# Performance work log

Hardware: AMD Instinct MI355X
Metric: run time of the kernel (lower is better)

The kernel has to match this reference:

```python
import jax, jax.numpy as jnp
import numpy as np
from jax import lax

EPS = 1e-05
Q = 4          # window size (hard-coded in BotBlock)
HEADS = 4
DIM = 16       # bottleneck(64) // heads(4)


def conv3x3(x, w, b):
    # x: [N,C,H,W], w: [O,I,3,3]
    y = lax.conv_general_dilated(x, w, (1, 1), ((1, 1), (1, 1)),
                                 dimension_numbers=('NCHW', 'OIHW', 'NCHW'))
    return y + b[None, :, None, None]


def batchnorm(x, gamma, beta):
    # training-mode BN: batch statistics over (N,H,W), biased variance
    m = jnp.mean(x, axis=(0, 2, 3), keepdims=True)
    v = jnp.var(x, axis=(0, 2, 3), keepdims=True)
    xn = (x - m) * lax.rsqrt(v + EPS)
    return xn * gamma[None, :, None, None] + beta[None, :, None, None]


def rel_to_abs(x):
    # x: [B, H, L, 2L-1] -> [B, H, L, L] via pad/reshape trick
    B, H, L, _ = x.shape
    x = jnp.pad(x, ((0, 0), (0, 0), (0, 0), (0, 1)))          # [B,H,L,2L]
    flat = x.reshape(B, H, -1)                                  # [B,H,2L*L]
    flat = jnp.pad(flat, ((0, 0), (0, 0), (0, L - 1)))
    final = flat.reshape(B, H, L + 1, 2 * L - 1)
    return final[:, :, :L, L - 1:]                              # [B,H,L,L]


def relative_logits_1d(q, rel_k, perm):
    # q: [b, n, h, w, d], rel_k: [2w-1, d]
    b, n, h, w, d = q.shape
    rl = jnp.einsum('bnhwd,md->bnhwm', q, rel_k)
    rl = rl.reshape(b, n * h, w, 2 * w - 1)
    rl = rel_to_abs(rl)                                         # [b, n*h, w, w]
    rl = rl.reshape(b, n, h, w, w)
    rl = jnp.broadcast_to(rl[:, :, :, None], (b, n, h, h, w, w))
    return jnp.transpose(rl, perm)


def rel_pos_attention(q, k, v, rel_w, rel_h):
    # q,k,v: [b, heads, h, w, d]
    b, n, h, w, d = q.shape
    q = q * (d ** -0.5)
    logits = jnp.einsum('bnhwd,bnpqd->bnhwpq', q, k)
    logits = logits + relative_logits_1d(q, rel_w, (0, 1, 2, 4, 3, 5))
    logits = logits + relative_logits_1d(jnp.transpose(q, (0, 1, 3, 2, 4)),
                                         rel_h, (0, 1, 4, 2, 5, 3))
    weights = jax.nn.softmax(logits.reshape(b, n, h, w, h * w), axis=-1)
    weights = weights.reshape(b, n, h, w, h, w)
    out = jnp.einsum('bnhwpq,bnpqd->bhwnd', weights, v)         # [b,h,w,n,d]
    return out.reshape(b, h, w, n * d)                          # fold heads


def setup_inputs() -> dict:
    key = jax.random.key(0)
    ks = jax.random.split(key, 16)
    C_in, C_bot, C_out = 64, 64, 256
    inp = {
        'x': jax.random.normal(ks[0], (2, C_in, 256, 256), jnp.float32),
        'conv1_w': jax.random.normal(ks[1], (C_bot, C_in, 3, 3), jnp.float32) * 0.05,
        'conv1_b': jnp.zeros((C_bot,), jnp.float32),
        'bn1_g': jnp.ones((C_bot,), jnp.float32),
        'bn1_b': jnp.zeros((C_bot,), jnp.float32),
        'wq': jax.random.normal(ks[2], (C_bot, HEADS, DIM), jnp.float32) * 0.01,
        'wk': jax.random.normal(ks[3], (C_bot, HEADS, DIM), jnp.float32) * 0.01,
        'wv': jax.random.normal(ks[4], (C_bot, HEADS, DIM), jnp.float32) * 0.01,
        'rel_w': jax.random.normal(ks[5], (2 * Q - 1, DIM), jnp.float32) * (DIM ** -0.5),
        'rel_h': jax.random.normal(ks[6], (2 * Q - 1, DIM), jnp.float32) * (DIM ** -0.5),
        'bn2_g': jnp.ones((C_bot,), jnp.float32),
        'bn2_b': jnp.zeros((C_bot,), jnp.float32),
        'conv3_w': jax.random.normal(ks[7], (C_out, C_bot, 3, 3), jnp.float32) * 0.05,
        'conv3_b': jnp.zeros((C_out,), jnp.float32),
        # NOTE: original init_zero=True zeros bn3 gamma; we randomize it so the
        # output (and gradients) are non-trivial for kernel correctness checks.
        'bn3_g': jax.random.normal(ks[8], (C_out,), jnp.float32),
        'bn3_b': jnp.zeros((C_out,), jnp.float32),
    }
    return inp


def reference(x, conv1_w, conv1_b, bn1_g, bn1_b, wq, wk, wv, rel_w, rel_h,
              bn2_g, bn2_b, conv3_w, conv3_b, bn3_g, bn3_b):
    N, C, H, W = x.shape
    P_h, P_w = H // Q, W // Q
    # raw memory reinterpretation into 4x4 blocks (matches torch .reshape)
    xb = x.reshape(N * P_h * P_w, C, Q, Q)
    out = jax.nn.relu(batchnorm(conv3x3(xb, conv1_w, conv1_b), bn1_g, bn1_b))
    # GroupPointWise projections: NCHW -> NHWC then einsum
    feat = jnp.transpose(out, (0, 2, 3, 1))                     # [b,h,w,c]
    q = jnp.einsum('bhwc,cnp->bnhwp', feat, wq)
    k = jnp.einsum('bhwc,cnp->bnhwp', feat, wk)
    v = jnp.einsum('bhwc,cnp->bnhwp', feat, wv)
    o = rel_pos_attention(q, k, v, rel_w, rel_h)                # [b,h,w,c]
    o = jnp.transpose(o, (0, 3, 1, 2))                          # NCHW
    o = jax.nn.relu(batchnorm(o, bn2_g, bn2_b))
    o = batchnorm(conv3x3(o, conv3_w, conv3_b), bn3_g, bn3_b)   # no act
    C1 = o.shape[1]
    o = o.reshape(N, C1, H, W)
    return jax.nn.relu(o)
```

## Files before the change

kernel.cpp:

```cpp
#include <hip/hip_runtime.h>
#include <stdint.h>


#define EPSV 1e-5f
#define INV_N (1.0f / 131072.0f)

typedef unsigned short u16;
typedef __attribute__((ext_vector_type(8))) short short8b;
typedef __attribute__((ext_vector_type(4))) float f32x4;

__device__ __forceinline__ u16 f2bf(float f) {
  unsigned u = __float_as_uint(f);
  u += 0x7fffu + ((u >> 16) & 1u);
  return (u16)(u >> 16);
}
__device__ __forceinline__ float bf2f(u16 h) {
  return __uint_as_float((unsigned)h << 16);
}
__device__ __forceinline__ unsigned cvtpk(float lo, float hi) {
  unsigned r;
  asm("v_cvt_pk_bf16_f32 %0, %1, %2" : "=v"(r) : "v"(lo), "v"(hi));
  return r;
}

__device__ __forceinline__ float bn_scale(const float* __restrict__ acc,
                                          const float* __restrict__ gam,
                                          const float* __restrict__ bet,
                                          int C, int c, float& shift) {
  float S = acc[c], S2 = acc[C + c];
  float mean = S * INV_N;
  float var  = S2 * INV_N - mean * mean;
  float rstd = rsqrtf(var + EPSV);
  float sc = gam[c] * rstd;
  shift = bet[c] - mean * sc;
  return sc;
}

__global__ __launch_bounds__(256) void prep_kernel(const float* __restrict__ w1,
                                                   const float* __restrict__ w3,
                                                   const float* __restrict__ wq,
                                                   const float* __restrict__ wk,
                                                   const float* __restrict__ wv,
                                                   const float* __restrict__ relw,
                                                   const float* __restrict__ relh,
                                                   u16* __restrict__ wp1,
                                                   u16* __restrict__ wp3,
                                                   u16* __restrict__ wqkvT) {
  int i = blockIdx.x * 256 + threadIdx.x;
  const int tot1 = 18 * 64 * 40;
  const int tot3 = 9 * 256 * 64;
  if (i < tot1) {
    int ch = i / (64 * 40); int r = i - ch * 64 * 40; int o = r / 40; int kk = r - o * 40;
    float v = 0.f;
    if (kk < 32) { int k = ch * 32 + kk; int tap = k >> 6; int c = k & 63;
                   v = w1[o * 576 + c * 9 + tap]; }
    wp1[i] = f2bf(v);
  } else if (i < tot1 + tot3) {
    int j = i - tot1;
    int tap = j >> 14; int r = j & 16383; int o = r >> 6; int c = r & 63;
    wp3[j] = f2bf(w3[o * 576 + c * 9 + tap]);
  } else if (i < tot1 + tot3 + 192 * 64) {
    int j = i - tot1 - tot3;
    int oc = j >> 6, c = j & 63;
    const float* src = (oc < 64) ? wq : (oc < 128) ? wk : wv;
    wqkvT[j] = f2bf(src[(c << 6) + (oc & 63)]);
  } else if (i < tot1 + tot3 + 192 * 64 + 4096) {
    int j = i - tot1 - tot3 - 192 * 64;
    int c = j & 63; int col = (j >> 6) & 31; int tbl = j >> 11;
    int n = col >> 3, m = col & 7;
    float v = 0.f;
    if (m < 7) {
      const float* rel = tbl ? relh : relw;
#pragma unroll
      for (int d = 0; d < 16; ++d) v += wq[c * 64 + n * 16 + d] * rel[m * 16 + d];
    }
    wqkvT[(192 + tbl * 32 + col) * 64 + c] = f2bf(v);
  }
}

__global__ __launch_bounds__(256) void conv1_kernel(const float* __restrict__ x,
                                                    const u16* __restrict__ wp,
                                                    u16* __restrict__ bufb,
                                                    float* __restrict__ partials1) {
  __shared__ __align__(16) char featA[257 * 128];
  __shared__ __align__(16) char ldsW[2][64 * 80];
  const int t = threadIdx.x;
  const int lane = t & 63, w = t >> 6;
  const int lrow = lane & 15, lk = lane >> 4;
  const int wm = w >> 1, wn = w & 1;
  const size_t Mbase = (size_t)blockIdx.x * 256;

  int rel[9];
  {
    const int pi = lrow >> 2, pj = lrow & 3;
#pragma unroll
    for (int tap = 0; tap < 9; ++tap) {
      const int ti = tap / 3, tj = tap - ti * 3;
      int si = pi + ti - 1, sj = pj + tj - 1;
      bool valid = ((unsigned)si < 4u) && ((unsigned)sj < 4u);
      rel[tap] = valid ? ((si * 4 + sj) << 7) : (1 << 24);
    }
  }

  {
    const int cp = t >> 3, ph = t & 7;
    const int gsw = ((cp >> 2) << 4) | ((cp & 3) << 2);
#pragma unroll
    for (int i = 0; i < 16; ++i) {
      const float* bp = x + Mbase * 64 + i * 1024 + cp * 32 + ph * 2;
      float2 a = *reinterpret_cast<const float2*>(bp);
      float2 b = *reinterpret_cast<const float2*>(bp + 16);
#pragma unroll
      for (int j = 0; j < 2; ++j) {
        const int row = i * 16 + ph * 2 + j;
        unsigned pk = cvtpk(j ? a.y : a.x, j ? b.y : b.x);
        const int byte = row * 128 + (gsw ^ ((row & 7) << 4));
        *reinterpret_cast<unsigned*>(featA + byte) = pk;
      }
    }
  }
  if (t < 8) *reinterpret_cast<uint4*>(featA + 256 * 128 + t * 16) = uint4{0, 0, 0, 0};

  uint4 s0, s1;
  {
    const u16* sp = wp;
    s0 = *reinterpret_cast<const uint4*>(sp + (size_t)t * 8);
    if (t < 64) s1 = *reinterpret_cast<const uint4*>(sp + (size_t)(t + 256) * 8);
    *reinterpret_cast<uint4*>(ldsW[0] + t * 16) = s0;
    if (t < 64) *reinterpret_cast<uint4*>(ldsW[0] + (t + 256) * 16) = s1;
  }
  __syncthreads();

  f32x4 acc[8][2] = {};
#pragma unroll
  for (int chn = 0; chn < 18; ++chn) {
    const int cur = chn & 1;
    const int tap = chn >> 1, kk = chn & 1;
    if (chn + 1 < 18) {
      const u16* sp = wp + (chn + 1) * 2560;
      s0 = *reinterpret_cast<const uint4*>(sp + (size_t)t * 8);
      if (t < 64) s1 = *reinterpret_cast<const uint4*>(sp + (size_t)(t + 256) * 8);
    }
    const int kkg = (kk << 6) | (lk << 4);
    short8b bw[2];
#pragma unroll
    for (int n = 0; n < 2; ++n)
      bw[n] = *reinterpret_cast<const short8b*>(ldsW[cur] + (wn * 32 + n * 16 + lrow) * 80 + lk * 16);
#pragma unroll
    for (int m = 0; m < 8; ++m) {
      int ad = ((wm * 128 + m * 16) << 7) + rel[tap];
      ad = ad < 32768 ? ad : 32768;
      ad += (kkg ^ ((ad >> 3) & 0x70));
      short8b af = *reinterpret_cast<const short8b*>(featA + ad);
#pragma unroll
      for (int n = 0; n < 2; ++n)
        acc[m][n] = __builtin_amdgcn_mfma_f32_16x16x32_bf16(af, bw[n], acc[m][n], 0, 0, 0);
    }
    if (chn + 1 < 18) {
      *reinterpret_cast<uint4*>(ldsW[cur ^ 1] + t * 16) = s0;
      if (t < 64) *reinterpret_cast<uint4*>(ldsW[cur ^ 1] + (t + 256) * 16) = s1;
    }
    __syncthreads();
  }

#pragma unroll
  for (int m = 0; m < 8; ++m) {
    const size_t rowg0 = Mbase + wm * 128 + m * 16 + lk * 4;
#pragma unroll
    for (int n = 0; n < 2; ++n) {
      const int o = wn * 32 + n * 16 + lrow;
#pragma unroll
      for (int r = 0; r < 4; ++r)
        bufb[(rowg0 + r) * 64 + o] = f2bf(acc[m][n][r]);
    }
  }

  float* pst = reinterpret_cast<float*>(featA);
  if (t < 128) pst[t] = 0.f;
  __syncthreads();
#pragma unroll
  for (int n = 0; n < 2; ++n) {
    float s = 0.f, s2 = 0.f;
#pragma unroll
    for (int m = 0; m < 8; ++m)
#pragma unroll
      for (int r = 0; r < 4; ++r) {
        float v = acc[m][n][r];
        s += v; s2 = fmaf(v, v, s2);
      }
    s += __shfl_xor(s, 16); s2 += __shfl_xor(s2, 16);
    s += __shfl_xor(s, 32); s2 += __shfl_xor(s2, 32);
    if (lk == 0) {
      const int o = wn * 32 + n * 16 + lrow;
      atomicAdd(&pst[o], s);
      atomicAdd(&pst[64 + o], s2);
    }
  }
  __syncthreads();
  if (t < 128) partials1[(size_t)blockIdx.x * 128 + t] = pst[t];
}

__global__ __launch_bounds__(256) void reduce12_kernel(const float* __restrict__ p,
                                                       float* __restrict__ acc, int nrows) {
  const int c = blockIdx.x, t = threadIdx.x;
  float s = 0.f;
  for (int i = t; i < nrows; i += 256) s += p[(size_t)i * 128 + c];
#pragma unroll
  for (int off = 32; off > 0; off >>= 1) s += __shfl_down(s, off);
  __shared__ float red[4];
  if ((t & 63) == 0) red[t >> 6] = s;
  __syncthreads();
  if (t == 0) acc[c] = red[0] + red[1] + red[2] + red[3];
}

__global__ __launch_bounds__(256) void attn_kernel(u16* __restrict__ buf,
                                                   const u16* __restrict__ wqkvT,
                                                   const float* __restrict__ acc1,
                                                   const float* __restrict__ g1,
                                                   const float* __restrict__ b1,
                                                   float* __restrict__ partials2) {
  __shared__ float scsh[64][2];
  __shared__ float pstA[128];
  __shared__ __align__(16) u16 feat_l[4][1024];
  __shared__ __align__(16) float qkvf[4][3200];
  __shared__ __align__(16) float relLs[4][1152];
  const int t = threadIdx.x, u = t >> 6, lane = t & 63;
  const size_t b = (size_t)blockIdx.x * 4 + u;
  float* Wf = qkvf[u];
  float* rL = relLs[u];

  if (t < 64) {
    float sh; float sc = bn_scale(acc1, g1, b1, 64, t, sh);
    scsh[t][0] = sc; scsh[t][1] = sh;
  }
  if (t < 128) pstA[t] = 0.f;
  __syncthreads();

  {
    const int pos = lane >> 2, cq = lane & 3;
    const u16* src = buf + b * 1024 + pos * 64 + cq * 16;
    short8b v0 = *reinterpret_cast<const short8b*>(src);
    short8b v1 = *reinterpret_cast<const short8b*>(src + 8);
    float f[16];
#pragma unroll
    for (int j = 0; j < 8; ++j) {
      const int c0 = cq * 16 + j, c1 = cq * 16 + 8 + j;
      f[j]     = fmaxf(fmaf(bf2f((u16)v0[j]), scsh[c0][0], scsh[c0][1]), 0.f);
      f[8 + j] = fmaxf(fmaf(bf2f((u16)v1[j]), scsh[c1][0], scsh[c1][1]), 0.f);
    }
    uint4 q0{cvtpk(f[0], f[1]), cvtpk(f[2], f[3]), cvtpk(f[4], f[5]), cvtpk(f[6], f[7])};
    uint4 q1{cvtpk(f[8], f[9]), cvtpk(f[10], f[11]), cvtpk(f[12], f[13]), cvtpk(f[14], f[15])};
    const int g0 = (cq * 2) ^ (pos & 7), g1g = (cq * 2 + 1) ^ (pos & 7);
    *reinterpret_cast<uint4*>(&feat_l[u][pos * 64 + g0 * 8]) = q0;
    *reinterpret_cast<uint4*>(&feat_l[u][pos * 64 + g1g * 8]) = q1;
  }

  const int dq = lane & 15, lk = lane >> 4;
  short8b afr[2];
#pragma unroll
  for (int ch = 0; ch < 2; ++ch) {
    const int kg = ch * 4 + lk;
    afr[ch] = *reinterpret_cast<const short8b*>(&feat_l[u][dq * 64 + ((kg ^ (dq & 7)) * 8)]);
  }
#pragma unroll
  for (int ct = 0; ct < 16; ++ct) {
    f32x4 d = {0.f, 0.f, 0.f, 0.f};
#pragma unroll
    for (int ch = 0; ch < 2; ++ch) {
      short8b bfr = *reinterpret_cast<const short8b*>(&wqkvT[(ct * 16 + dq) * 64 + ch * 32 + lk * 8]);
      d = __builtin_amdgcn_mfma_f32_16x16x32_bf16(afr[ch], bfr, d, 0, 0, 0);
    }
    if (ct < 4) {
      float* dst = Wf + ct * 272;
#pragma unroll
      for (int r = 0; r < 4; ++r) dst[(lk * 4 + r) * 17 + dq] = d[r] * 0.25f;
    } else if (ct < 12) {
      float* dst = (ct < 8) ? (Wf + 1088 + (ct - 4) * 264) : (Wf + 2144 + (ct - 8) * 264);
      const int cp = dq ^ (lk << 2);
#pragma unroll
      for (int r = 0; r < 4; ++r) dst[(lk * 4 + r) * 16 + cp] = d[r];
    } else {
      const int rc = ct - 12, tbl = rc >> 1;
      const int nn = ((rc & 1) << 1) | (dq >> 3), mm = dq & 7;
      float* dst = rL + tbl * 576 + nn * 144 + mm;
#pragma unroll
      for (int r = 0; r < 4; ++r) dst[(lk * 4 + r) * 9] = d[r] * 0.25f;
    }
  }

  const int n = lk, qp = dq;
  const int qi = qp >> 2, qj = qp & 3;
  float q_[16];
  {
    const float* qb = Wf + n * 272 + qp * 17;
#pragma unroll
    for (int d2 = 0; d2 < 16; ++d2) q_[d2] = qb[d2];
  }
  float rwq[4], rhq[4];
  {
    const float* rw = rL + n * 144 + qp * 9 + (3 - qj);
    const float* rh = rL + 576 + n * 144 + qp * 9 + (3 - qi);
#pragma unroll
    for (int k = 0; k < 4; ++k) { rwq[k] = rw[k]; rhq[k] = rh[k]; }
  }
  float lo[16]; float mx = -1e30f;
  const float* kbase = Wf + 1088 + n * 264;
#pragma unroll
  for (int kp = 0; kp < 16; ++kp) {
    const float4* kr = reinterpret_cast<const float4*>(kbase + kp * 16);
    float s = rwq[kp & 3] + rhq[kp >> 2];
#pragma unroll
    for (int g = 0; g < 4; ++g) {
      float4 kv = kr[g];
      const int lg = (g ^ (kp >> 2)) * 4;
      s = fmaf(q_[lg], kv.x, s); s = fmaf(q_[lg + 1], kv.y, s);
      s = fmaf(q_[lg + 2], kv.z, s); s = fmaf(q_[lg + 3], kv.w, s);
    }
    lo[kp] = s; mx = fmaxf(mx, s);
  }
  float ssum = 0.f;
#pragma unroll
  for (int kp = 0; kp < 16; ++kp) { float e = __expf(lo[kp] - mx); lo[kp] = e; ssum += e; }
  const float inv = 1.0f / ssum;
  float ov[16];
#pragma unroll
  for (int j = 0; j < 16; ++j) ov[j] = 0.f;
  const float* vbase = Wf + 2144 + n * 264;
#pragma unroll
  for (int kp = 0; kp < 16; ++kp) {
    const float4* vr = reinterpret_cast<const float4*>(vbase + kp * 16);
    const float wgt = lo[kp];
#pragma unroll
    for (int g = 0; g < 4; ++g) {
      float4 vv = vr[g];
      const int lg = (g ^ (kp >> 2)) * 4;
      ov[lg] = fmaf(wgt, vv.x, ov[lg]);
      ov[lg + 1] = fmaf(wgt, vv.y, ov[lg + 1]);
      ov[lg + 2] = fmaf(wgt, vv.z, ov[lg + 2]);
      ov[lg + 3] = fmaf(wgt, vv.w, ov[lg + 3]);
    }
  }
#pragma unroll
  for (int j = 0; j < 16; ++j) ov[j] *= inv;

  {
    uint4 o0{cvtpk(ov[0], ov[1]), cvtpk(ov[2], ov[3]), cvtpk(ov[4], ov[5]), cvtpk(ov[6], ov[7])};
    uint4 o1{cvtpk(ov[8], ov[9]), cvtpk(ov[10], ov[11]), cvtpk(ov[12], ov[13]), cvtpk(ov[14], ov[15])};
    u16* dstb = buf + b * 1024 + qp * 64 + (n << 4);
    *reinterpret_cast<uint4*>(dstb) = o0;
    *reinterpret_cast<uint4*>(dstb + 8) = o1;
  }

  {
    float* fl = Wf;
#pragma unroll
    for (int j = 0; j < 16; ++j) fl[qp * 69 + n * 16 + j] = ov[j];
    const int c = lane;
    float s = 0.f, s2 = 0.f;
#pragma unroll
    for (int pos = 0; pos < 16; ++pos) {
      float v = fl[pos * 69 + c];
      s += v; s2 = fmaf(v, v, s2);
    }
    atomicAdd(&pstA[c], s);
    atomicAdd(&pstA[64 + c], s2);
  }
  __syncthreads();
  if (t < 128) partials2[(size_t)blockIdx.x * 128 + t] = pstA[t];
}

__global__ __launch_bounds__(256, 2) void conv3_kernel(const u16* __restrict__ src,
                                                       const u16* __restrict__ wp,
                                                       const float* __restrict__ acc2,
                                                       const float* __restrict__ g2,
                                                       const float* __restrict__ b2,
                                                       u16* __restrict__ y3b,
                                                       float* __restrict__ partials3) {
  __shared__ __align__(16) u16 featB[257 * 64];
  __shared__ __align__(16) u16 ldsW[2][128 * 64];
  __shared__ float scsh[128];
  const int t = threadIdx.x;
  const int lane = t & 63, w = t >> 6;
  const int lrow = lane & 15, lk = lane >> 4;
  const int wm = w >> 1, wn = w & 1;
  const int Nbase = blockIdx.x * 256;
  const int ohalf = blockIdx.y;

  int rel[9];
  {
    const int pi = lrow >> 2, pj = lrow & 3;
#pragma unroll
    for (int tap = 0; tap < 9; ++tap) {
      const int ti = tap / 3, tj = tap - ti * 3;
      int si = pi + ti - 1, sj = pj + tj - 1;
      bool valid = ((unsigned)si < 4u) && ((unsigned)sj < 4u);
      rel[tap] = valid ? ((si * 4 + sj) << 7) : (1 << 24);
    }
  }
  if (t < 64) {
    float sh; float sc = bn_scale(acc2, g2, b2, 64, t, sh);
    scsh[t * 2] = sc; scsh[t * 2 + 1] = sh;
  }
  const int so = t >> 1, shalf = t & 1, so7 = so & 7;
  {
    const u16* wsrc = wp + ohalf * 8192 + so * 64 + shalf * 32;
    uint4 w0 = *reinterpret_cast<const uint4*>(wsrc);
    uint4 w1 = *reinterpret_cast<const uint4*>(wsrc + 8);
    uint4 w2 = *reinterpret_cast<const uint4*>(wsrc + 16);
    uint4 w3v = *reinterpret_cast<const uint4*>(wsrc + 24);
    char* dst = (char*)ldsW[0] + so * 128;
    const int gb = shalf * 4;
    *reinterpret_cast<uint4*>(dst + (((gb + 0) ^ so7) << 4)) = w0;
    *reinterpret_cast<uint4*>(dst + (((gb + 1) ^ so7) << 4)) = w1;
    *reinterpret_cast<uint4*>(dst + (((gb + 2) ^ so7) << 4)) = w2;
    *reinterpret_cast<uint4*>(dst + (((gb + 3) ^ so7) << 4)) = w3v;
  }
  __syncthreads();
  {
    const u16* srow = src + (size_t)(Nbase + t) * 64;
    char* drow = (char*)featB + t * 128;
    const int r7 = t & 7;
#pragma unroll
    for (int g = 0; g < 8; ++g) {
      short8b v = *reinterpret_cast<const short8b*>(srow + g * 8);
      float f[8];
#pragma unroll
      for (int j = 0; j < 8; ++j) {
        const int c = g * 8 + j;
        f[j] = fmaxf(fmaf(bf2f((u16)v[j]), scsh[c * 2], scsh[c * 2 + 1]), 0.f);
      }
      uint4 pk{cvtpk(f[0], f[1]), cvtpk(f[2], f[3]), cvtpk(f[4], f[5]), cvtpk(f[6], f[7])};
      *reinterpret_cast<uint4*>(drow + ((g ^ r7) << 4)) = pk;
    }
  }
  if (t < 8) *reinterpret_cast<uint4*>((char*)featB + 32768 + t * 16) = uint4{0, 0, 0, 0};
  uint4 r0, r1, r2, r3v;
  {
    const u16* wsrc = wp + 16384 + ohalf * 8192 + so * 64 + shalf * 32;
    r0 = *reinterpret_cast<const uint4*>(wsrc);
    r1 = *reinterpret_cast<const uint4*>(wsrc + 8);
    r2 = *reinterpret_cast<const uint4*>(wsrc + 16);
    r3v = *reinterpret_cast<const uint4*>(wsrc + 24);
  }
  __syncthreads();
  f32x4 acc[4][8] = {};
  const char* fB = (const char*)featB;
  const int swzA0 = (lk << 4) ^ ((lrow & 7) << 4);
  const int swzA1 = (64 | (lk << 4)) ^ ((lrow & 7) << 4);
#pragma unroll
  for (int tap = 0; tap < 9; ++tap) {
    const int cur = tap & 1;
    const char* lW = (const char*)ldsW[cur];
    short8b aw0[4], aw1[4];
#pragma unroll
    for (int m = 0; m < 4; ++m) {
      const int rowoff = (wm * 64 + m * 16 + lrow) << 7;
      aw0[m] = *reinterpret_cast<const short8b*>(lW + rowoff + swzA0);
      aw1[m] = *reinterpret_cast<const short8b*>(lW + rowoff + swzA1);
    }
#pragma unroll
    for (int n = 0; n < 8; ++n) {
      int ad0 = ((wn * 128 + n * 16) << 7) + rel[tap];
      ad0 = ad0 < 32768 ? ad0 : 32768;
      const int swz = (ad0 >> 3) & 0x70;
      short8b bf0 = *reinterpret_cast<const short8b*>(fB + ad0 + ((lk << 4) ^ swz));
      short8b bf1 = *reinterpret_cast<const short8b*>(fB + ad0 + ((64 | (lk << 4)) ^ swz));
#pragma unroll
      for (int m = 0; m < 4; ++m) {
        acc[m][n] = __builtin_amdgcn_mfma_f32_16x16x32_bf16(aw0[m], bf0, acc[m][n], 0, 0, 0);
        acc[m][n] = __builtin_amdgcn_mfma_f32_16x16x32_bf16(aw1[m], bf1, acc[m][n], 0, 0, 0);
      }
    }
    if (tap < 8) {
      char* dst = (char*)ldsW[cur ^ 1] + so * 128;
      const int gb = shalf * 4;
      *reinterpret_cast<uint4*>(dst + (((gb + 0) ^ so7) << 4)) = r0;
      *reinterpret_cast<uint4*>(dst + (((gb + 1) ^ so7) << 4)) = r1;
      *reinterpret_cast<uint4*>(dst + (((gb + 2) ^ so7) << 4)) = r2;
      *reinterpret_cast<uint4*>(dst + (((gb + 3) ^ so7) << 4)) = r3v;
      if (tap < 7) {
        const u16* wsrc = wp + (tap + 2) * 16384 + ohalf * 8192 + so * 64 + shalf * 32;
        r0 = *reinterpret_cast<const uint4*>(wsrc);
        r1 = *reinterpret_cast<const uint4*>(wsrc + 8);
        r2 = *reinterpret_cast<const uint4*>(wsrc + 16);
        r3v = *reinterpret_cast<const uint4*>(wsrc + 24);
      }
    }
    __syncthreads();
  }
#pragma unroll
  for (int m = 0; m < 4; ++m) {
    const int o = ohalf * 128 + wm * 64 + m * 16 + lk * 4;
#pragma unroll
    for (int n = 0; n < 8; ++n) {
      const int colg = Nbase + wn * 128 + n * 16 + lrow;
      const int b = colg >> 4, p = colg & 15;
      u16* dst = y3b + (size_t)b * 4096 + (size_t)o * 16 + p;
#pragma unroll
      for (int r = 0; r < 4; ++r) dst[r * 16] = f2bf(acc[m][n][r]);
    }
  }
  float* pst = reinterpret_cast<float*>(featB);
  pst[t] = 0.f;
  __syncthreads();
#pragma unroll
  for (int m = 0; m < 4; ++m) {
#pragma unroll
    for (int r = 0; r < 4; ++r) {
      float s = 0.f, s2 = 0.f;
#pragma unroll
      for (int n = 0; n < 8; ++n) {
        float v = acc[m][n][r];
        s += v; s2 = fmaf(v, v, s2);
      }
      s += __shfl_xor(s, 1); s2 += __shfl_xor(s2, 1);
      s += __shfl_xor(s, 2); s2 += __shfl_xor(s2, 2);
      s += __shfl_xor(s, 4); s2 += __shfl_xor(s2, 4);
      s += __shfl_xor(s, 8); s2 += __shfl_xor(s2, 8);
      if (lrow == 0) {
        const int ch = wm * 64 + m * 16 + lk * 4 + r;
        atomicAdd(&pst[ch], s);
        atomicAdd(&pst[128 + ch], s2);
      }
    }
  }
  __syncthreads();
  partials3[((size_t)(ohalf * 512 + blockIdx.x)) * 256 + t] = pst[t];
}

__global__ __launch_bounds__(256) void reduce3_kernel(const float* __restrict__ p,
                                                      float* __restrict__ acc3) {
  const int c2 = blockIdx.x, t = threadIdx.x;
  const int kind = c2 >> 8, c = c2 & 255;
  const int h = c >> 7, chl = c & 127;
  float s = 0.f;
  for (int i = t; i < 512; i += 256)
    s += p[((size_t)(h * 512 + i)) * 256 + kind * 128 + chl];
#pragma unroll
  for (int off = 32; off > 0; off >>= 1) s += __shfl_down(s, off);
  __shared__ float red[4];
  if ((t & 63) == 0) red[t >> 6] = s;
  __syncthreads();
  if (t == 0) acc3[kind * 256 + c] = red[0] + red[1] + red[2] + red[3];
}

__global__ __launch_bounds__(256) void final_kernel(const u16* __restrict__ y3b,
                                                    float* __restrict__ out,
                                                    const float* __restrict__ acc3,
                                                    const float* __restrict__ g3,
                                                    const float* __restrict__ b3) {
  const size_t i = ((size_t)blockIdx.x * 256 + threadIdx.x) * 8;
  const int c = (int)((i >> 4) & 255);
  float sh; const float sc = bn_scale(acc3, g3, b3, 256, c, sh);
  short8b v = *reinterpret_cast<const short8b*>(y3b + i);
  float4 o0, o1;
  o0.x = fmaxf(fmaf(bf2f((u16)v[0]), sc, sh), 0.f);
  o0.y = fmaxf(fmaf(bf2f((u16)v[1]), sc, sh), 0.f);
  o0.z = fmaxf(fmaf(bf2f((u16)v[2]), sc, sh), 0.f);
  o0.w = fmaxf(fmaf(bf2f((u16)v[3]), sc, sh), 0.f);
  o1.x = fmaxf(fmaf(bf2f((u16)v[4]), sc, sh), 0.f);
  o1.y = fmaxf(fmaf(bf2f((u16)v[5]), sc, sh), 0.f);
  o1.z = fmaxf(fmaf(bf2f((u16)v[6]), sc, sh), 0.f);
  o1.w = fmaxf(fmaf(bf2f((u16)v[7]), sc, sh), 0.f);
  *reinterpret_cast<float4*>(out + i) = o0;
  *reinterpret_cast<float4*>(out + i + 4) = o1;
}

extern "C" void kernel_launch(void* const* d_in, const int* in_sizes, int n_in,
                              void* d_out, int out_size, void* d_ws, size_t ws_size,
                              hipStream_t stream) {
  const float* x   = (const float*)d_in[0];
  const float* w1  = (const float*)d_in[1];
  const float* g1  = (const float*)d_in[3];
  const float* bb1 = (const float*)d_in[4];
  const float* wq  = (const float*)d_in[5];
  const float* wk  = (const float*)d_in[6];
  const float* wv  = (const float*)d_in[7];
  const float* rw  = (const float*)d_in[8];
  const float* rh  = (const float*)d_in[9];
  const float* g2  = (const float*)d_in[10];
  const float* bb2 = (const float*)d_in[11];
  const float* w3  = (const float*)d_in[12];
  const float* g3  = (const float*)d_in[14];
  const float* bb3 = (const float*)d_in[15];
  float* out = (float*)d_out;
  float* ws  = (float*)d_ws;

  u16*   bufb   = (u16*)ws;
  u16*   y3     = bufb + 8388608;
  u16*   wp1    = y3 + 33554432;
  u16*   wp3    = wp1 + 46080;
  u16*   wqkvT  = wp3 + 147456;
  float* acc1   = ws + 21076480;
  float* acc2   = acc1 + 128;
  float* acc3   = acc2 + 128;
  float* part1  = acc3 + 512;
  float* part2  = part1 + 65536;
  float* part3  = part2 + 262144;

  prep_kernel<<<820, 256, 0, stream>>>(w1, w3, wq, wk, wv, rw, rh, wp1, wp3, wqkvT);
  conv1_kernel<<<512, 256, 0, stream>>>(x, wp1, bufb, part1);
  reduce12_kernel<<<128, 256, 0, stream>>>(part1, acc1, 512);
  attn_kernel<<<2048, 256, 0, stream>>>(bufb, wqkvT, acc1, g1, bb1, part2);
  reduce12_kernel<<<128, 256, 0, stream>>>(part2, acc2, 2048);
  conv3_kernel<<<dim3(512, 2), 256, 0, stream>>>(bufb, wp3, acc2, g2, bb2, y3, part3);
  reduce3_kernel<<<512, 256, 0, stream>>>(part3, acc3);
  final_kernel<<<16384, 256, 0, stream>>>(y3, out, acc3, g3, bb3);
}
```

Baseline: 159.9 us.

## Compute attention QK and PV with MFMA and keep Q/K/V in registers

The attention kernel now computes the 16x16 QK^T logits and the PV product per head with 16x16x16 bf16 MFMA instructions, replacing per-lane scalar FMA loops. Q, K and V fragments stay in registers as bf16 instead of being staged through large fp32 LDS buffers, and softmax reductions use cross-lane shuffles. The 0.25 query scale is folded into the precomputed weights in the prep kernel. This cuts LDS footprint and VALU work, at the cost of bf16 rounding of Q/K/V, the probabilities and the relative logits.

```diff
diff --git a/kernel.cpp b/kernel.cpp
--- a/kernel.cpp
+++ b/kernel.cpp
@@ -7,6 +7,7 @@
 
 typedef unsigned short u16;
 typedef __attribute__((ext_vector_type(8))) short short8b;
+typedef __attribute__((ext_vector_type(4))) short short4b;
 typedef __attribute__((ext_vector_type(4))) float f32x4;
 
 __device__ __forceinline__ u16 f2bf(float f) {
@@ -21,6 +22,23 @@
   unsigned r;
   asm("v_cvt_pk_bf16_f32 %0, %1, %2" : "=v"(r) : "v"(lo), "v"(hi));
   return r;
+}
+__device__ __forceinline__ short4b pack4(unsigned lo, unsigned hi) {
+  union { unsigned u[2]; short4b s; } x;
+  x.u[0] = lo; x.u[1] = hi;
+  return x.s;
+}
+__device__ __forceinline__ f32x4 mfma16(short4b a, short4b b, f32x4 c) {
+#if __has_builtin(__builtin_amdgcn_mfma_f32_16x16x16_bf16)
+  return __builtin_amdgcn_mfma_f32_16x16x16_bf16(a, b, c, 0, 0, 0);
+#elif __has_builtin(__builtin_amdgcn_mfma_f32_16x16x16bf16_1k)
+  return __builtin_amdgcn_mfma_f32_16x16x16bf16_1k(a, b, c, 0, 0, 0);
+#else
+  f32x4 d;
+  asm volatile("v_mfma_f32_16x16x16_bf16 %0, %1, %2, %3\n\ts_nop 7\n\ts_nop 7"
+               : "=v"(d) : "v"(a), "v"(b), "v"(c));
+  return d;
+#endif
 }
 
 __device__ __forceinline__ float bn_scale(const float* __restrict__ acc,
@@ -63,7 +81,9 @@
     int j = i - tot1 - tot3;
     int oc = j >> 6, c = j & 63;
     const float* src = (oc < 64) ? wq : (oc < 128) ? wk : wv;
-    wqkvT[j] = f2bf(src[(c << 6) + (oc & 63)]);
+    float v = src[(c << 6) + (oc & 63)];
+    if (oc < 64) v *= 0.25f;
+    wqkvT[j] = f2bf(v);
   } else if (i < tot1 + tot3 + 192 * 64 + 4096) {
     int j = i - tot1 - tot3 - 192 * 64;
     int c = j & 63; int col = (j >> 6) & 31; int tbl = j >> 11;
@@ -73,6 +93,7 @@
       const float* rel = tbl ? relh : relw;
 #pragma unroll
       for (int d = 0; d < 16; ++d) v += wq[c * 64 + n * 16 + d] * rel[m * 16 + d];
+      v *= 0.25f;
     }
     wqkvT[(192 + tbl * 32 + col) * 64 + c] = f2bf(v);
   }
@@ -222,12 +243,17 @@
   __shared__ float scsh[64][2];
   __shared__ float pstA[128];
   __shared__ __align__(16) u16 feat_l[4][1024];
-  __shared__ __align__(16) float qkvf[4][3200];
-  __shared__ __align__(16) float relLs[4][1152];
+  __shared__ __align__(16) float S_lds[4][16 * 18];
+  __shared__ __align__(16) u16 V_lds[4][16 * 20];
+  __shared__ __align__(16) float inv_lds[4][16];
+  __shared__ __align__(16) u16 rLs[4][1152];
   const int t = threadIdx.x, u = t >> 6, lane = t & 63;
   const size_t b = (size_t)blockIdx.x * 4 + u;
-  float* Wf = qkvf[u];
-  float* rL = relLs[u];
+  const int lrow = lane & 15, lk = lane >> 4;
+  float* Sl = S_lds[u];
+  u16* Vl = V_lds[u];
+  float* invl = inv_lds[u];
+  u16* rL = rLs[u];
 
   if (t < 64) {
     float sh; float sc = bn_scale(acc1, g1, b1, 64, t, sh);
@@ -255,115 +281,81 @@
     *reinterpret_cast<uint4*>(&feat_l[u][pos * 64 + g1g * 8]) = q1;
   }
 
-  const int dq = lane & 15, lk = lane >> 4;
-  short8b afr[2];
+  short8b bfeat[2];
 #pragma unroll
   for (int ch = 0; ch < 2; ++ch) {
     const int kg = ch * 4 + lk;
-    afr[ch] = *reinterpret_cast<const short8b*>(&feat_l[u][dq * 64 + ((kg ^ (dq & 7)) * 8)]);
-  }
+    bfeat[ch] = *reinterpret_cast<const short8b*>(&feat_l[u][lrow * 64 + ((kg ^ (lrow & 7)) * 8)]);
+  }
+  short4b qf[4], kf[4];
+  uint2 vf[4];
 #pragma unroll
   for (int ct = 0; ct < 16; ++ct) {
     f32x4 d = {0.f, 0.f, 0.f, 0.f};
 #pragma unroll
     for (int ch = 0; ch < 2; ++ch) {
-      short8b bfr = *reinterpret_cast<const short8b*>(&wqkvT[(ct * 16 + dq) * 64 + ch * 32 + lk * 8]);
-      d = __builtin_amdgcn_mfma_f32_16x16x32_bf16(afr[ch], bfr, d, 0, 0, 0);
+      short8b wfr = *reinterpret_cast<const short8b*>(&wqkvT[(ct * 16 + lrow) * 64 + ch * 32 + lk * 8]);
+      d = __builtin_amdgcn_mfma_f32_16x16x32_bf16(wfr, bfeat[ch], d, 0, 0, 0);
     }
     if (ct < 4) {
-      float* dst = Wf + ct * 272;
-#pragma unroll
-      for (int r = 0; r < 4; ++r) dst[(lk * 4 + r) * 17 + dq] = d[r] * 0.25f;
+      qf[ct] = pack4(cvtpk(d[0], d[1]), cvtpk(d[2], d[3]));
+    } else if (ct < 8) {
+      kf[ct - 4] = pack4(cvtpk(d[0], d[1]), cvtpk(d[2], d[3]));
     } else if (ct < 12) {
-      float* dst = (ct < 8) ? (Wf + 1088 + (ct - 4) * 264) : (Wf + 2144 + (ct - 8) * 264);
-      const int cp = dq ^ (lk << 2);
-#pragma unroll
-      for (int r = 0; r < 4; ++r) dst[(lk * 4 + r) * 16 + cp] = d[r];
+      vf[ct - 8] = uint2{cvtpk(d[0], d[1]), cvtpk(d[2], d[3])};
     } else {
-      const int rc = ct - 12, tbl = rc >> 1;
-      const int nn = ((rc & 1) << 1) | (dq >> 3), mm = dq & 7;
-      float* dst = rL + tbl * 576 + nn * 144 + mm;
-#pragma unroll
-      for (int r = 0; r < 4; ++r) dst[(lk * 4 + r) * 9] = d[r] * 0.25f;
-    }
-  }
-
-  const int n = lk, qp = dq;
-  const int qi = qp >> 2, qj = qp & 3;
-  float q_[16];
-  {
-    const float* qb = Wf + n * 272 + qp * 17;
-#pragma unroll
-    for (int d2 = 0; d2 < 16; ++d2) q_[d2] = qb[d2];
-  }
-  float rwq[4], rhq[4];
-  {
-    const float* rw = rL + n * 144 + qp * 9 + (3 - qj);
-    const float* rh = rL + 576 + n * 144 + qp * 9 + (3 - qi);
-#pragma unroll
-    for (int k = 0; k < 4; ++k) { rwq[k] = rw[k]; rhq[k] = rh[k]; }
-  }
-  float lo[16]; float mx = -1e30f;
-  const float* kbase = Wf + 1088 + n * 264;
-#pragma unroll
-  for (int kp = 0; kp < 16; ++kp) {
-    const float4* kr = reinterpret_cast<const float4*>(kbase + kp * 16);
-    float s = rwq[kp & 3] + rhq[kp >> 2];
-#pragma unroll
-    for (int g = 0; g < 4; ++g) {
-      float4 kv = kr[g];
-      const int lg = (g ^ (kp >> 2)) * 4;
-      s = fmaf(q_[lg], kv.x, s); s = fmaf(q_[lg + 1], kv.y, s);
-      s = fmaf(q_[lg + 2], kv.z, s); s = fmaf(q_[lg + 3], kv.w, s);
-    }
-    lo[kp] = s; mx = fmaxf(mx, s);
-  }
-  float ssum = 0.f;
-#pragma unroll
-  for (int kp = 0; kp < 16; ++kp) { float e = __expf(lo[kp] - mx); lo[kp] = e; ssum += e; }
-  const float inv = 1.0f / ssum;
-  float ov[16];
-#pragma unroll
-  for (int j = 0; j < 16; ++j) ov[j] = 0.f;
-  const float* vbase = Wf + 2144 + n * 264;
-#pragma unroll
-  for (int kp = 0; kp < 16; ++kp) {
-    const float4* vr = reinterpret_cast<const float4*>(vbase + kp * 16);
-    const float wgt = lo[kp];
-#pragma unroll
-    for (int g = 0; g < 4; ++g) {
-      float4 vv = vr[g];
-      const int lg = (g ^ (kp >> 2)) * 4;
-      ov[lg] = fmaf(wgt, vv.x, ov[lg]);
-      ov[lg + 1] = fmaf(wgt, vv.y, ov[lg + 1]);
-      ov[lg + 2] = fmaf(wgt, vv.z, ov[lg + 2]);
-      ov[lg + 3] = fmaf(wgt, vv.w, ov[lg + 3]);
-    }
-  }
-#pragma unroll
-  for (int j = 0; j < 16; ++j) ov[j] *= inv;
-
-  {
-    uint4 o0{cvtpk(ov[0], ov[1]), cvtpk(ov[2], ov[3]), cvtpk(ov[4], ov[5]), cvtpk(ov[6], ov[7])};
-    uint4 o1{cvtpk(ov[8], ov[9]), cvtpk(ov[10], ov[11]), cvtpk(ov[12], ov[13]), cvtpk(ov[14], ov[15])};
-    u16* dstb = buf + b * 1024 + qp * 64 + (n << 4);
-    *reinterpret_cast<uint4*>(dstb) = o0;
-    *reinterpret_cast<uint4*>(dstb + 8) = o1;
-  }
-
-  {
-    float* fl = Wf;
-#pragma unroll
-    for (int j = 0; j < 16; ++j) fl[qp * 69 + n * 16 + j] = ov[j];
-    const int c = lane;
-    float s = 0.f, s2 = 0.f;
-#pragma unroll
-    for (int pos = 0; pos < 16; ++pos) {
-      float v = fl[pos * 69 + c];
-      s += v; s2 = fmaf(v, v, s2);
-    }
-    atomicAdd(&pstA[c], s);
-    atomicAdd(&pstA[64 + c], s2);
+#pragma unroll
+      for (int r = 0; r < 4; ++r) {
+        const int rc = (ct - 12) * 16 + lk * 4 + r;
+        const int tbl = rc >> 5, col = rc & 31;
+        rL[tbl * 576 + (col >> 3) * 144 + lrow * 9 + (col & 7)] = f2bf(d[r]);
+      }
+    }
+  }
+
+  const f32x4 fzero = {0.f, 0.f, 0.f, 0.f};
+  const int qj3 = 3 - (lrow & 3);
+  const int qi = lrow >> 2;
+#pragma unroll
+  for (int n = 0; n < 4; ++n) {
+    f32x4 S = mfma16(qf[n], kf[n], fzero);
+#pragma unroll
+    for (int r = 0; r < 4; ++r) Sl[(lk * 4 + r) * 18 + lrow] = S[r];
+    const float* srow = Sl + lrow * 18 + lk * 4;
+    float2 sa = *reinterpret_cast<const float2*>(srow);
+    float2 sb = *reinterpret_cast<const float2*>(srow + 2);
+    float s0 = sa.x, s1 = sa.y, s2 = sb.x, s3 = sb.y;
+    const u16* rwp = rL + n * 144 + lrow * 9 + qj3;
+    const float rh = bf2f(rL[576 + n * 144 + lrow * 9 + 3 + lk - qi]);
+    s0 += bf2f(rwp[0]) + rh; s1 += bf2f(rwp[1]) + rh;
+    s2 += bf2f(rwp[2]) + rh; s3 += bf2f(rwp[3]) + rh;
+    float m = fmaxf(fmaxf(s0, s1), fmaxf(s2, s3));
+    m = fmaxf(m, __shfl_xor(m, 16)); m = fmaxf(m, __shfl_xor(m, 32));
+    float p0 = __expf(s0 - m), p1 = __expf(s1 - m);
+    float p2 = __expf(s2 - m), p3 = __expf(s3 - m);
+    float ls = p0 + p1 + p2 + p3;
+    ls += __shfl_xor(ls, 16); ls += __shfl_xor(ls, 32);
+    if (lk == 0) invl[lrow] = 1.f / ls;
+    short4b pf = pack4(cvtpk(p0, p1), cvtpk(p2, p3));
+    *reinterpret_cast<uint2*>(Vl + lrow * 20 + lk * 4) = vf[n];
+    const int vb = lk * 4;
+    unsigned v0 = Vl[(vb + 0) * 20 + lrow], v1 = Vl[(vb + 1) * 20 + lrow];
+    unsigned v2 = Vl[(vb + 2) * 20 + lrow], v3 = Vl[(vb + 3) * 20 + lrow];
+    short4b vB = pack4(v0 | (v1 << 16), v2 | (v3 << 16));
+    f32x4 O = mfma16(pf, vB, fzero);
+    float4 iv = *reinterpret_cast<const float4*>(invl + lk * 4);
+    float o0 = O[0] * iv.x, o1 = O[1] * iv.y, o2 = O[2] * iv.z, o3 = O[3] * iv.w;
+    u16* ob = buf + b * 1024 + (n << 4) + lrow;
+    ob[(lk * 4 + 0) * 64] = f2bf(o0); ob[(lk * 4 + 1) * 64] = f2bf(o1);
+    ob[(lk * 4 + 2) * 64] = f2bf(o2); ob[(lk * 4 + 3) * 64] = f2bf(o3);
+    float ss = o0 + o1 + o2 + o3;
+    float s2s = o0 * o0 + o1 * o1 + o2 * o2 + o3 * o3;
+    ss += __shfl_xor(ss, 16); s2s += __shfl_xor(s2s, 16);
+    ss += __shfl_xor(ss, 32); s2s += __shfl_xor(s2s, 32);
+    if (lk == 0) {
+      atomicAdd(&pstA[(n << 4) + lrow], ss);
+      atomicAdd(&pstA[64 + (n << 4) + lrow], s2s);
+    }
   }
   __syncthreads();
   if (t < 128) partials2[(size_t)blockIdx.x * 128 + t] = pstA[t];
```

After: 156.5 us, median of 2. 1.02x faster.
